# Kernel optimization log

Hardware: AMD Instinct MI355X
Metric: run time of the kernel (lower is better)

The kernel has to match this reference:

```python
import jax, jax.numpy as jnp
import numpy as np

SPARSITY = 0.15
GAIN = 3.0

def setup_inputs() -> dict:
    key = jax.random.key(0)
    x = jax.random.normal(key, (16384, 4096), dtype=jnp.float32)
    return {"x": x}

def reference(x):
    N, D = x.shape
    k = max(int(D * SPARSITY), 2)
    topk_values, topk_indices = jax.lax.top_k(x, k)  # [N, k]
    diff = topk_values[:, 0] - topk_values[:, 1]      # [N]
    dynamic_gain = (jax.nn.sigmoid(diff) * GAIN + 1.0)[:, None]  # [N, 1]
    rows = jnp.arange(N)[:, None]
    mask = jnp.zeros_like(x).at[rows, topk_indices].set(1.0)
    return x * mask * dynamic_gain
```

## Files before the change

### kernel.cpp

```cpp
#include <hip/hip_runtime.h>
#include <math.h>


#define D     4096
#define K     614
#define BLOCK 256
#define VPT   64
#define NB    16

__device__ __forceinline__ unsigned int f2ord(float f) {
    unsigned int b = __float_as_uint(f);
    return (b & 0x80000000u) ? ~b : (b | 0x80000000u);
}
__device__ __forceinline__ float ord2f(unsigned int u) {
    unsigned int b = (u & 0x80000000u) ? (u ^ 0x80000000u) : ~u;
    return __uint_as_float(b);
}

__global__ __launch_bounds__(BLOCK, 5)
void diffgated_topk(const float* __restrict__ x, float* __restrict__ out, int rows) {
    const int lane = threadIdx.x & 63;
    const int wav  = threadIdx.x >> 6;
    const int row  = blockIdx.x * 4 + wav;
    if (row >= rows) return;
    const float* xrow = x + (size_t)row * D;
    float*       orow = out + (size_t)row * D;

    unsigned int u[VPT];
    float m1 = -INFINITY, m2 = -INFINITY;
    #pragma unroll
    for (int b = 0; b < NB; ++b) {
        float4 v = ((const float4*)xrow)[b * 64 + lane];
        float vs[4] = { v.x, v.y, v.z, v.w };
        #pragma unroll
        for (int j = 0; j < 4; ++j) {
            float f = vs[j];
            if (f > m1) { m2 = m1; m1 = f; } else if (f > m2) { m2 = f; }
            u[b * 4 + j] = f2ord(f);
        }
    }

    #pragma unroll
    for (int off = 32; off; off >>= 1) {
        float o1 = __shfl_xor(m1, off);
        float o2 = __shfl_xor(m2, off);
        float hi = fmaxf(m1, o1), lo2 = fminf(m1, o1);
        m2 = fmaxf(lo2, fmaxf(m2, o2));
        m1 = hi;
    }
    const float gain = 1.0f / (1.0f + expf(-(m1 - m2))) * 3.0f + 1.0f;

    unsigned long long lo = 0ull, hi = 0x100000000ull;
    for (int it = 0; it < 32; ++it) {
        unsigned int mid = (unsigned int)((lo + hi) >> 1);
        int cnt = 0;
        #pragma unroll
        for (int j = 0; j < VPT; ++j)
            cnt += (int)__popcll(__ballot(u[j] >= mid));
        if (cnt >= K) lo = mid; else hi = mid;
    }
    const unsigned int ut = (unsigned int)lo;

    int cnt_gt = 0, cnt_eq = 0;
    #pragma unroll
    for (int j = 0; j < VPT; ++j) {
        cnt_gt += (int)__popcll(__ballot(u[j] >  ut));
        cnt_eq += (int)__popcll(__ballot(u[j] == ut));
    }
    const int needed = K - cnt_gt;

    if (cnt_eq == needed) {
        #pragma unroll
        for (int b = 0; b < NB; ++b) {
            float4 o; float* op = (float*)&o;
            #pragma unroll
            for (int j = 0; j < 4; ++j) {
                unsigned int uu = u[b * 4 + j];
                op[j] = (uu >= ut) ? ord2f(uu) * gain : 0.0f;
            }
            ((float4*)orow)[b * 64 + lane] = o;
        }
    } else {
        const unsigned long long ltmask =
            (lane == 0) ? 0ull : ((~0ull) >> (64 - lane));
        int eq_before = 0;
        #pragma unroll
        for (int b = 0; b < NB; ++b) {
            unsigned long long bal[4];
            #pragma unroll
            for (int j = 0; j < 4; ++j) bal[j] = __ballot(u[b * 4 + j] == ut);
            float4 o; float* op = (float*)&o;
            #pragma unroll
            for (int j = 0; j < 4; ++j) {
                unsigned int uu = u[b * 4 + j];
                float f = 0.0f;
                if (uu > ut) {
                    f = ord2f(uu) * gain;
                } else if (uu == ut) {
                    int r = eq_before;
                    #pragma unroll
                    for (int j2 = 0; j2 < 4; ++j2) {
                        r += (int)__popcll(bal[j2] & ltmask);
                        if (j2 < j) r += (int)((bal[j2] >> lane) & 1ull);
                    }
                    if (r < needed) f = ord2f(uu) * gain;
                }
                op[j] = f;
            }
            ((float4*)orow)[b * 64 + lane] = o;
            #pragma unroll
            for (int j2 = 0; j2 < 4; ++j2)
                eq_before += (int)__popcll(bal[j2]);
        }
    }
}

extern "C" void kernel_launch(void* const* d_in, const int* in_sizes, int n_in,
                              void* d_out, int out_size, void* d_ws, size_t ws_size,
                              hipStream_t stream) {
    const float* x = (const float*)d_in[0];
    float* out = (float*)d_out;
    const int rows = in_sizes[0] / D;
    diffgated_topk<<<dim3((rows + 3) / 4), dim3(BLOCK), 0, stream>>>(x, out, rows);
}
```

Baseline: 530.5 us.

## Exit radix bisection early on exact count and use nontemporal stores

```diff
diff --git a/kernel.cpp b/kernel.cpp
--- a/kernel.cpp
+++ b/kernel.cpp
@@ -8,79 +8,77 @@
 #define VPT   64
 #define NB    16
 
+typedef float f32x4 __attribute__((ext_vector_type(4)));
+
 __device__ __forceinline__ unsigned int f2ord(float f) {
     unsigned int b = __float_as_uint(f);
-    return (b & 0x80000000u) ? ~b : (b | 0x80000000u);
+    return ((int)b >= 0) ? (b | 0x80000000u) : ~b;
 }
 __device__ __forceinline__ float ord2f(unsigned int u) {
-    unsigned int b = (u & 0x80000000u) ? (u ^ 0x80000000u) : ~u;
-    return __uint_as_float(b);
+    return __uint_as_float(((int)u < 0) ? (u ^ 0x80000000u) : ~u);
 }
 
-__global__ __launch_bounds__(BLOCK, 5)
+__global__ __launch_bounds__(BLOCK, 4)
 void diffgated_topk(const float* __restrict__ x, float* __restrict__ out, int rows) {
     const int lane = threadIdx.x & 63;
     const int wav  = threadIdx.x >> 6;
     const int row  = blockIdx.x * 4 + wav;
     if (row >= rows) return;
-    const float* xrow = x + (size_t)row * D;
-    float*       orow = out + (size_t)row * D;
+    const f32x4* xrow = (const f32x4*)(x + (size_t)row * D);
+    f32x4*       orow = (f32x4*)(out + (size_t)row * D);
 
     unsigned int u[VPT];
-    float m1 = -INFINITY, m2 = -INFINITY;
+    unsigned int m1 = 0u, m2 = 0u;
     #pragma unroll
     for (int b = 0; b < NB; ++b) {
-        float4 v = ((const float4*)xrow)[b * 64 + lane];
-        float vs[4] = { v.x, v.y, v.z, v.w };
+        f32x4 v = xrow[b * 64 + lane];
         #pragma unroll
         for (int j = 0; j < 4; ++j) {
-            float f = vs[j];
-            if (f > m1) { m2 = m1; m1 = f; } else if (f > m2) { m2 = f; }
-            u[b * 4 + j] = f2ord(f);
+            unsigned int q = f2ord(v[j]);
+            unsigned int lo2 = min(m1, q);
+            m1 = max(m1, q);
+            m2 = max(m2, lo2);
+            u[b * 4 + j] = q;
         }
     }
 
     #pragma unroll
     for (int off = 32; off; off >>= 1) {
-        float o1 = __shfl_xor(m1, off);
-        float o2 = __shfl_xor(m2, off);
-        float hi = fmaxf(m1, o1), lo2 = fminf(m1, o1);
-        m2 = fmaxf(lo2, fmaxf(m2, o2));
-        m1 = hi;
+        unsigned int o1 = __shfl_xor(m1, off);
+        unsigned int o2 = __shfl_xor(m2, off);
+        unsigned int hi2 = max(m1, o1), lo2 = min(m1, o1);
+        m2 = max(m2, max(lo2, o2));
+        m1 = hi2;
     }
-    const float gain = 1.0f / (1.0f + expf(-(m1 - m2))) * 3.0f + 1.0f;
+    const float gain = 3.0f / (1.0f + expf(-(ord2f(m1) - ord2f(m2)))) + 1.0f;
 
     unsigned long long lo = 0ull, hi = 0x100000000ull;
-    for (int it = 0; it < 32; ++it) {
+    int cnt_lo = D, cnt_hi = 0;
+    while (hi - lo > 1ull) {
         unsigned int mid = (unsigned int)((lo + hi) >> 1);
         int cnt = 0;
         #pragma unroll
         for (int j = 0; j < VPT; ++j)
             cnt += (int)__popcll(__ballot(u[j] >= mid));
-        if (cnt >= K) lo = mid; else hi = mid;
+        if (cnt >= K) { lo = mid; cnt_lo = cnt; if (cnt == K) break; }
+        else          { hi = mid; cnt_hi = cnt; }
     }
     const unsigned int ut = (unsigned int)lo;
+    const float g = gain;
 
-    int cnt_gt = 0, cnt_eq = 0;
-    #pragma unroll
-    for (int j = 0; j < VPT; ++j) {
-        cnt_gt += (int)__popcll(__ballot(u[j] >  ut));
-        cnt_eq += (int)__popcll(__ballot(u[j] == ut));
-    }
-    const int needed = K - cnt_gt;
-
-    if (cnt_eq == needed) {
+    if (cnt_lo == K) {
         #pragma unroll
         for (int b = 0; b < NB; ++b) {
-            float4 o; float* op = (float*)&o;
+            f32x4 o;
             #pragma unroll
             for (int j = 0; j < 4; ++j) {
                 unsigned int uu = u[b * 4 + j];
-                op[j] = (uu >= ut) ? ord2f(uu) * gain : 0.0f;
+                o[j] = (uu >= ut) ? ord2f(uu) * g : 0.0f;
             }
-            ((float4*)orow)[b * 64 + lane] = o;
+            __builtin_nontemporal_store(o, orow + b * 64 + lane);
         }
     } else {
+        const int needed = K - cnt_hi;
         const unsigned long long ltmask =
             (lane == 0) ? 0ull : ((~0ull) >> (64 - lane));
         int eq_before = 0;
@@ -89,13 +87,13 @@
             unsigned long long bal[4];
             #pragma unroll
             for (int j = 0; j < 4; ++j) bal[j] = __ballot(u[b * 4 + j] == ut);
-            float4 o; float* op = (float*)&o;
+            f32x4 o;
             #pragma unroll
             for (int j = 0; j < 4; ++j) {
                 unsigned int uu = u[b * 4 + j];
                 float f = 0.0f;
                 if (uu > ut) {
-                    f = ord2f(uu) * gain;
+                    f = ord2f(uu) * g;
                 } else if (uu == ut) {
                     int r = eq_before;
                     #pragma unroll
@@ -103,11 +101,11 @@
                         r += (int)__popcll(bal[j2] & ltmask);
                         if (j2 < j) r += (int)((bal[j2] >> lane) & 1ull);
                     }
-                    if (r < needed) f = ord2f(uu) * gain;
+                    if (r < needed) f = ord2f(uu) * g;
                 }
-                op[j] = f;
+                o[j] = f;
             }
-            ((float4*)orow)[b * 64 + lane] = o;
+            __builtin_nontemporal_store(o, orow + b * 64 + lane);
             #pragma unroll
             for (int j2 = 0; j2 < 4; ++j2)
                 eq_before += (int)__popcll(bal[j2]);
```

After: 471.7 us. 1.12x faster.
